# Optimization experiments

Measured on AMD Instinct MI355X. Metric: run time of the kernel, lower is better.

Reference implementation:

```python
import jax, jax.numpy as jnp
import numpy as np

K = 8192          # codebook_size
D = 256           # embedding_dim
BETA = 0.25
DECAY = 0.99
EPS = 1e-5        # EMA eps


def setup_inputs() -> dict:
    key = jax.random.key(0)
    k1, k2 = jax.random.split(key)
    z_e = jax.random.normal(k1, (16, D, 32, 32), dtype=jnp.float32)
    # nn.init.uniform_(weight, -1/K, 1/K)
    weight = jax.random.uniform(k2, (K, D), dtype=jnp.float32, minval=-1.0 / K, maxval=1.0 / K)
    cluster_size = jnp.zeros((K,), dtype=jnp.float32)
    embed_avg = jnp.zeros((K, D), dtype=jnp.float32)
    return {"z_e": z_e, "weight": weight, "cluster_size": cluster_size, "embed_avg": embed_avg}


def reference(z_e, weight, cluster_size, embed_avg):
    B, Dd, H, W = z_e.shape
    flat = z_e.transpose(0, 2, 3, 1).reshape(-1, Dd)          # [N, D]
    codebook = jax.lax.stop_gradient(weight)                    # [K, D]

    # squared L2 distances via expansion (same math as torch source)
    x_sq = jnp.sum(flat * flat, axis=1, keepdims=True)          # [N, 1]
    e_sq = jnp.sum(codebook * codebook, axis=1)[None, :]        # [1, K]
    cross = flat @ codebook.T                                   # [N, K] GEMM
    dist = x_sq + e_sq - 2.0 * cross
    indices = jnp.argmin(dist, axis=1)                          # [N]

    N = flat.shape[0]
    # EMA update (one-hot scatter expressed as segment ops)
    counts = jax.ops.segment_sum(jnp.ones((N,), flat.dtype), indices, num_segments=K)
    embed_sum = jax.ops.segment_sum(flat, indices, num_segments=K)   # [K, D]
    new_cluster = cluster_size * DECAY + counts * (1.0 - DECAY)
    new_embed_avg = embed_avg * DECAY + embed_sum * (1.0 - DECAY)
    n = jnp.sum(new_cluster)
    cs = (new_cluster + EPS) / (n + K * EPS) * n
    new_weight = new_embed_avg / cs[:, None]                    # updated codebook

    # quantize: gather from the UPDATED codebook (as in the torch forward order)
    e = new_weight[indices]                                     # [N, D]
    z_q = e.reshape(B, H, W, Dd).transpose(0, 3, 1, 2)

    commitment_loss = BETA * jnp.mean((z_e - jax.lax.stop_gradient(z_q)) ** 2)
    codebook_loss = jnp.mean((z_q - jax.lax.stop_gradient(z_e)) ** 2)
    usage = counts / N
    return (z_q, commitment_loss, codebook_loss, usage, new_cluster, new_embed_avg)
```

## Files before the change

kernel.cpp:

```cpp
#include <hip/hip_runtime.h>
#include <cstdint>
#include <cstddef>

#define N_TOK   16384
#define K_CODE  8192
#define D_DIM   256
#define HW      1024
#define MARGIN  8e-4f
#define RING    512
#define CAP     990

#define OFF_ZQ   0
#define OFF_CL   4194304
#define OFF_CBL  4194305
#define OFF_USE  4194306
#define OFF_NC   4202498
#define OFF_AVG  4210690

typedef unsigned short ushort_t;
typedef __attribute__((ext_vector_type(8))) short short8;
typedef __attribute__((ext_vector_type(8))) unsigned short ushort8;
typedef __attribute__((ext_vector_type(4))) float f32x4;

__device__ float g_esq[K_CODE];
__device__ float g_xsq[N_TOK];
__device__ __attribute__((aligned(16))) float    g_xf[N_TOK * D_DIM];
__device__ __attribute__((aligned(16))) ushort_t g_xb[N_TOK * D_DIM];
__device__ __attribute__((aligned(16))) ushort_t g_wb[K_CODE * D_DIM];
__device__ int   g_ccnt[N_TOK];
__device__ int   g_cand[N_TOK * RING];
__device__ int   g_idx[N_TOK];
__device__ float g_cnt[K_CODE];
__device__ __attribute__((aligned(16))) float g_esum[K_CODE * D_DIM];
__device__ float g_inv[K_CODE];
__device__ float g_loss[1];

__device__ __forceinline__ ushort_t f2bf(float f) {
  unsigned u = __builtin_bit_cast(unsigned, f);
  return (ushort_t)((u + 0x7FFFu + ((u >> 16) & 1u)) >> 16);
}

__device__ __forceinline__ void gload16(const void* g, void* l) {
  __builtin_amdgcn_global_load_lds(
      (const __attribute__((address_space(1))) unsigned int*)g,
      (__attribute__((address_space(3))) unsigned int*)l, 16, 0, 0);
}

__global__ void k_zero() {
  int i = blockIdx.x * 256 + threadIdx.x;
  if (i < K_CODE) g_cnt[i] = 0.0f;
  if (i < N_TOK) g_ccnt[i] = 0;
  if (i == 0) g_loss[0] = 0.0f;
  for (int j = i; j < K_CODE * D_DIM; j += 524288) g_esum[j] = 0.0f;
}

__global__ void k_esq(const float* __restrict__ wt) {
  int t = threadIdx.x;
  int code = blockIdx.x * 4 + (t >> 6);
  int l = t & 63;
  float4 v = *(const float4*)(wt + (size_t)code * D_DIM + l * 4);
  float s = v.x * v.x + v.y * v.y + v.z * v.z + v.w * v.w;
  #pragma unroll
  for (int m = 1; m < 64; m <<= 1) s += __shfl_xor(s, m, 64);
  if (l == 0) g_esq[code] = s;
}

__global__ void k_split_w(const float* __restrict__ wt) {
  int tg = blockIdx.x * 256 + threadIdx.x;
  int c = tg >> 5, g = tg & 31;
  const float* src = wt + (size_t)c * D_DIM + g * 8;
  float4 v0 = *(const float4*)(src);
  float4 v1 = *(const float4*)(src + 4);
  ushort8 v;
  v[0] = f2bf(v0.x); v[1] = f2bf(v0.y); v[2] = f2bf(v0.z); v[3] = f2bf(v0.w);
  v[4] = f2bf(v1.x); v[5] = f2bf(v1.y); v[6] = f2bf(v1.z); v[7] = f2bf(v1.w);
  *(ushort8*)(g_wb + (size_t)c * D_DIM + ((g ^ (c & 7)) << 3)) = v;
}

__global__ __launch_bounds__(256) void k_prep_x(const float* __restrict__ ze) {
  extern __shared__ char smem[];
  float* T = (float*)smem;
  const int tid = threadIdx.x;
  const int n0 = blockIdx.x * 64;
  const int b = n0 >> 10, hw0 = n0 & 1023;
  const float* zb = ze + (size_t)b * (D_DIM * HW) + hw0;
  #pragma unroll
  for (int p = 0; p < 16; ++p) {
    int idx = p * 256 + tid;
    int d = idx >> 4, f = idx & 15;
    float4 v = *(const float4*)(zb + (size_t)d * HW + f * 4);
    T[(f * 4 + 0) * 260 + d] = v.x;
    T[(f * 4 + 1) * 260 + d] = v.y;
    T[(f * 4 + 2) * 260 + d] = v.z;
    T[(f * 4 + 3) * 260 + d] = v.w;
  }
  __syncthreads();
  if (tid < 64) {
    #pragma clang fp contract(off)
    float s = 0.0f;
    const float* tr = T + tid * 260;
    for (int d = 0; d < D_DIM; ++d) { float v = tr[d]; s = s + v * v; }
    g_xsq[n0 + tid] = s;
  }
  {
    int r = tid >> 2, dc = (tid & 3) * 64;
    const float* tr = T + r * 260 + dc;
    float* dst = g_xf + (size_t)(n0 + r) * D_DIM + dc;
    #pragma unroll
    for (int j = 0; j < 16; ++j) *(float4*)(dst + j * 4) = *(const float4*)(tr + j * 4);
  }
  {
    int r = tid >> 2, gb = (tid & 3) * 8;
    const float* tr = T + r * 260;
    ushort_t* dst = g_xb + (size_t)(n0 + r) * D_DIM;
    int swz = r & 7;
    #pragma unroll
    for (int gg = 0; gg < 8; ++gg) {
      int g = gb + gg;
      ushort8 v;
      #pragma unroll
      for (int j = 0; j < 8; ++j) v[j] = f2bf(tr[g * 8 + j]);
      *(ushort8*)(dst + ((g ^ swz) << 3)) = v;
    }
  }
}

__global__ __launch_bounds__(256, 1) void k_approx1() {
  extern __shared__ char smem[];
  ushort_t* As = (ushort_t*)smem;
  ushort_t* Bs = (ushort_t*)(smem + 32768);
  int* lcnt = (int*)(smem + 65536);

  const int tid = threadIdx.x;
  const int lane = tid & 63, wid = tid >> 6;
  const int col = lane & 15, kg = lane >> 4;
  const int rb = blockIdx.x & 255, sp = blockIdx.x >> 8;
  const int sw = col & 7;
  int* lbuf = (int*)(smem + 65552 + wid * 3960);

  if (tid < 4) lcnt[tid] = 0;

  {
    const char* s = (const char*)g_xb + (size_t)rb * 32768 + wid * 1024 + lane * 16;
    char* d = smem + wid * 1024;
    #pragma unroll
    for (int it = 0; it < 8; ++it) gload16(s + it * 4096, d + it * 4096);
  }
  const char* wsrc = (const char*)g_wb + (size_t)sp * (4096 * 512);
  {
    const char* s = wsrc + wid * 1024 + lane * 16;
    char* d = smem + 32768 + wid * 1024;
    #pragma unroll
    for (int it = 0; it < 4; ++it) gload16(s + it * 4096, d + it * 4096);
  }

  const int rowbase = rb * 64 + wid * 16 + (kg << 2);
  float rm[4], thr[4];
  #pragma unroll
  for (int r = 0; r < 4; ++r) { rm[r] = -1e30f; thr[r] = 1e30f; }

  __syncthreads();

  const int ar0 = (wid * 16 + col) * 256;
  #pragma unroll 1
  for (int ch = 0; ch < 128; ++ch) {
    const int cur = ch & 1;
    const int c0 = sp * 4096 + ch * 32;
    float e0 = g_esq[c0 + col];
    float e1 = g_esq[c0 + 16 + col];
    if (ch < 127) {
      const char* s = wsrc + (size_t)(ch + 1) * 16384 + wid * 1024 + lane * 16;
      char* d = smem + 32768 + ((cur ^ 1) << 14) + wid * 1024;
      #pragma unroll
      for (int it = 0; it < 4; ++it) gload16(s + it * 4096, d + it * 4096);
    }
    const ushort_t* Bb = Bs + (cur << 13);
    f32x4 acc0 = {0.f, 0.f, 0.f, 0.f};
    f32x4 acc1 = {0.f, 0.f, 0.f, 0.f};

    #pragma unroll
    for (int ks = 0; ks < 8; ++ks) {
      const int ko = ((ks * 4 + kg) ^ sw) << 3;
      short8 a  = *(const short8*)(As + ar0 + ko);
      short8 b0 = *(const short8*)(Bb + (col +  0) * 256 + ko);
      short8 b1 = *(const short8*)(Bb + (col + 16) * 256 + ko);
      acc0 = __builtin_amdgcn_mfma_f32_16x16x32_bf16(a, b0, acc0, 0, 0, 0);
      acc1 = __builtin_amdgcn_mfma_f32_16x16x32_bf16(a, b1, acc1, 0, 0, 0);
    }

    float cm[4];
    #pragma unroll
    for (int r = 0; r < 4; ++r) cm[r] = -1e30f;
    #pragma unroll
    for (int n = 0; n < 2; ++n) {
      const int c = c0 + n * 16 + col;
      const float e = n ? e1 : e0;
      const f32x4& a4 = n ? acc1 : acc0;
      #pragma unroll
      for (int r = 0; r < 4; ++r) {
        float sc = fmaf(2.0f, a4[r], -e);
        cm[r] = fmaxf(cm[r], sc);
        if (ch > 0 && sc >= thr[r]) {
          int row = rowbase + r;
          int pos = atomicAdd(&lcnt[wid], 1);
          if (pos < CAP) lbuf[pos] = (row << 13) | c;
          else { int gp = atomicAdd(&g_ccnt[row], 1);
                 if (gp < RING) g_cand[row * RING + gp] = c; }
        }
      }
    }
    #pragma unroll
    for (int mk = 1; mk < 16; mk <<= 1)
      #pragma unroll
      for (int r = 0; r < 4; ++r)
        cm[r] = fmaxf(cm[r], __shfl_xor(cm[r], mk, 64));
    #pragma unroll
    for (int r = 0; r < 4; ++r) {
      rm[r] = fmaxf(rm[r], cm[r]);
      thr[r] = rm[r] - MARGIN;
    }
    if (ch == 0) {
      #pragma unroll
      for (int n = 0; n < 2; ++n) {
        const int c = c0 + n * 16 + col;
        const float e = n ? e1 : e0;
        const f32x4& a4 = n ? acc1 : acc0;
        #pragma unroll
        for (int r = 0; r < 4; ++r) {
          float sc = fmaf(2.0f, a4[r], -e);
          if (sc >= thr[r]) {
            int row = rowbase + r;
            int pos = atomicAdd(&lcnt[wid], 1);
            if (pos < CAP) lbuf[pos] = (row << 13) | c;
            else { int gp = atomicAdd(&g_ccnt[row], 1);
                   if (gp < RING) g_cand[row * RING + gp] = c; }
          }
        }
      }
    }
    __syncthreads();
  }

  __syncthreads();
  int k = lcnt[wid];
  if (k > CAP) k = CAP;
  for (int i = lane; i < k; i += 64) {
    int e = lbuf[i];
    int row = e >> 13, c = e & 8191;
    int pos = atomicAdd(&g_ccnt[row], 1);
    if (pos < RING) g_cand[row * RING + pos] = c;
  }
}

__global__ __launch_bounds__(256) void k_rescore(const float* __restrict__ wt) {
  const int tid = threadIdx.x;
  const int lane = tid & 63, wid = tid >> 6;
  const int n = blockIdx.x * 4 + wid;
  const int grp = lane >> 4;
  const int l15 = lane & 15;
  float4 xf[4];
  const float* xr = g_xf + (size_t)n * D_DIM + l15 * 16;
  #pragma unroll
  for (int j = 0; j < 4; ++j) xf[j] = *(const float4*)(xr + j * 4);
  const float xsq = g_xsq[n];
  const int cnt = g_ccnt[n];
  float bd = INFINITY;
  int bi = 0x7fffffff;

  auto eval4 = [&](int c, bool active) {
    float p = 0.0f;
    if (active) {
      const float* wr = wt + (size_t)c * D_DIM + l15 * 16;
      #pragma unroll
      for (int j = 0; j < 4; ++j) {
        float4 w = *(const float4*)(wr + j * 4);
        p = fmaf(xf[j].x, w.x, p);
        p = fmaf(xf[j].y, w.y, p);
        p = fmaf(xf[j].z, w.z, p);
        p = fmaf(xf[j].w, w.w, p);
      }
    }
    #pragma unroll
    for (int m = 1; m < 16; m <<= 1) p += __shfl_xor(p, m, 64);
    if (active) {
      float d = (xsq + g_esq[c]) - 2.0f * p;
      if (d < bd || (d == bd && c < bi)) { bd = d; bi = c; }
    }
  };

  if (cnt >= 1 && cnt <= RING) {
    for (int i = 0; i < cnt; i += 4) {
      int idx = i + grp;
      bool act = idx < cnt;
      int c = act ? g_cand[n * RING + idx] : 0;
      eval4(c, act);
    }
  } else {
    for (int c0 = 0; c0 < K_CODE; c0 += 4) eval4(c0 + grp, true);
  }
  #pragma unroll
  for (int m = 16; m < 64; m <<= 1) {
    float od = __shfl_xor(bd, m, 64);
    int   oi = __shfl_xor(bi, m, 64);
    if (od < bd || (od == bd && oi < bi)) { bd = od; bi = oi; }
  }
  if (lane == 0) g_idx[n] = bi;
}

__global__ void k_scatter(const float* __restrict__ ze) {
  __shared__ int codes[64];
  int t = threadIdx.x;
  int n0 = blockIdx.x * 64;
  int b = n0 >> 10, hw0 = n0 & 1023;
  if (t < 64) {
    int c = g_idx[n0 + t];
    codes[t] = c;
    atomicAdd(&g_cnt[c], 1.0f);
  }
  __syncthreads();
  int f = t & 15, dd = t >> 4;
  const float* zb = ze + (size_t)b * (D_DIM * HW) + hw0;
  for (int p = 0; p < 16; ++p) {
    int d = p * 16 + dd;
    float4 v = *(const float4*)(zb + (size_t)d * HW + f * 4);
    atomicAdd(&g_esum[codes[4 * f + 0] * D_DIM + d], v.x);
    atomicAdd(&g_esum[codes[4 * f + 1] * D_DIM + d], v.y);
    atomicAdd(&g_esum[codes[4 * f + 2] * D_DIM + d], v.z);
    atomicAdd(&g_esum[codes[4 * f + 3] * D_DIM + d], v.w);
  }
}

__global__ void k_ema(const float* __restrict__ cs_in, float* __restrict__ out) {
  __shared__ float red[4];
  int t = threadIdx.x;
  float local = 0.0f;
  for (int k = t; k < K_CODE; k += 256) local += cs_in[k] * 0.99f + g_cnt[k] * 0.01f;
  #pragma unroll
  for (int m = 1; m < 64; m <<= 1) local += __shfl_xor(local, m, 64);
  if ((t & 63) == 0) red[t >> 6] = local;
  __syncthreads();
  float n = red[0] + red[1] + red[2] + red[3];
  float denom = n + 0.08192f;
  for (int k = t; k < K_CODE; k += 256) {
    float newc = cs_in[k] * 0.99f + g_cnt[k] * 0.01f;
    out[OFF_NC + k]  = newc;
    out[OFF_USE + k] = g_cnt[k] * (1.0f / 16384.0f);
    float cs = ((newc + 1e-5f) / denom) * n;
    g_inv[k] = 1.0f / cs;
  }
}

__global__ void k_avg(const float* __restrict__ ea, float* __restrict__ out) {
  int i = blockIdx.x * 256 + threadIdx.x;
  const float2 a = *(const float2*)(ea + (size_t)i * 2);
  const float2 s = *(const float2*)(g_esum + (size_t)i * 2);
  float2 o;
  o.x = a.x * 0.99f + s.x * 0.01f;
  o.y = a.y * 0.99f + s.y * 0.01f;
  *(float2*)(out + OFF_AVG + (size_t)i * 2) = o;
}

__global__ __launch_bounds__(256) void k_gather(const float* __restrict__ ze,
                                                float* __restrict__ out) {
  __shared__ float W[32 * 260];
  __shared__ int codes[64];
  __shared__ float red[4];
  const float* avg = out + OFF_AVG;
  int t = threadIdx.x;
  int n0 = blockIdx.x * 64;
  int b = n0 >> 10, hw0 = n0 & 1023;
  if (t < 64) codes[t] = g_idx[n0 + t];
  float l = 0.0f;
  const float* zb = ze + (size_t)b * (D_DIM * HW);
  float* qb = out + OFF_ZQ + (size_t)b * (D_DIM * HW);
  for (int pass = 0; pass < 2; ++pass) {
    __syncthreads();
    {
      int rr0 = t >> 6;
      int f = t & 63;
      for (int q = 0; q < 8; ++q) {
        int rr = q * 4 + rr0;
        int c = codes[pass * 32 + rr];
        float iv = g_inv[c];
        float2 w0 = *(const float2*)(avg + (size_t)c * D_DIM + f * 4);
        float2 w1 = *(const float2*)(avg + (size_t)c * D_DIM + f * 4 + 2);
        float* wp = &W[rr * 260 + f * 4];
        wp[0] = w0.x * iv; wp[1] = w0.y * iv; wp[2] = w1.x * iv; wp[3] = w1.y * iv;
      }
    }
    __syncthreads();
    int f = t & 7, dd = t >> 3;
    int hwp = hw0 + pass * 32;
    for (int p = 0; p < 8; ++p) {
      int d = p * 32 + dd;
      float4 zev = *(const float4*)(zb + (size_t)d * HW + hwp + f * 4);
      float4 o;
      o.x = W[(4 * f + 0) * 260 + d];
      o.y = W[(4 * f + 1) * 260 + d];
      o.z = W[(4 * f + 2) * 260 + d];
      o.w = W[(4 * f + 3) * 260 + d];
      *(float4*)(qb + (size_t)d * HW + hwp + f * 4) = o;
      float dx = zev.x - o.x, dy = zev.y - o.y, dz = zev.z - o.z, dw = zev.w - o.w;
      l += dx * dx; l += dy * dy; l += dz * dz; l += dw * dw;
    }
  }
  #pragma unroll
  for (int m = 1; m < 64; m <<= 1) l += __shfl_xor(l, m, 64);
  if ((t & 63) == 0) red[t >> 6] = l;
  __syncthreads();
  if (t == 0) atomicAdd(g_loss, red[0] + red[1] + red[2] + red[3]);
}

__global__ void k_final(float* __restrict__ out) {
  if (threadIdx.x == 0) {
    float mse = g_loss[0] * (1.0f / 4194304.0f);
    out[OFF_CL]  = 0.25f * mse;
    out[OFF_CBL] = mse;
  }
}

extern "C" void kernel_launch(void* const* d_in, const int* in_sizes, int n_in,
                              void* d_out, int out_size, void* d_ws, size_t ws_size,
                              hipStream_t stream) {
  const float* ze    = (const float*)d_in[0];
  const float* wt    = (const float*)d_in[1];
  const float* cs_in = (const float*)d_in[2];
  const float* ea_in = (const float*)d_in[3];
  float* out = (float*)d_out;
  (void)in_sizes; (void)n_in; (void)out_size; (void)d_ws; (void)ws_size;

  (void)hipFuncSetAttribute((const void*)k_prep_x,
                            hipFuncAttributeMaxDynamicSharedMemorySize, 66560);
  (void)hipFuncSetAttribute((const void*)k_approx1,
                            hipFuncAttributeMaxDynamicSharedMemorySize, 81408);

  k_zero<<<2048, 256, 0, stream>>>();
  k_esq<<<K_CODE / 4, 256, 0, stream>>>(wt);
  k_split_w<<<1024, 256, 0, stream>>>(wt);
  k_prep_x<<<N_TOK / 64, 256, 66560, stream>>>(ze);
  k_approx1<<<512, 256, 81408, stream>>>();
  k_rescore<<<N_TOK / 4, 256, 0, stream>>>(wt);
  k_scatter<<<N_TOK / 64, 256, 0, stream>>>(ze);
  k_ema<<<1, 256, 0, stream>>>(cs_in, out);
  k_avg<<<4096, 256, 0, stream>>>(ea_in, out);
  k_gather<<<N_TOK / 64, 256, 0, stream>>>(ze, out);
  k_final<<<1, 64, 0, stream>>>(out);
}
```

Baseline: 463.4 us.

## Hold A fragments in registers and double rows per block in approx GEMM

The approximate distance kernel now keeps each wave's 32 token rows as bf16 MFMA fragments in registers instead of LDS. Each block covers 128 tokens and 2048 codes, so every codebook tile loaded into LDS feeds twice as many MFMAs. The codebook traffic per block halves and LDS use drops. In exchange the kernel needs more VGPRs (16 short8 fragments plus 4 accumulators) and does more per-chunk threshold and shuffle work.

```diff
diff --git a/kernel.cpp b/kernel.cpp
--- a/kernel.cpp
+++ b/kernel.cpp
@@ -127,115 +127,137 @@
 
 __global__ __launch_bounds__(256, 1) void k_approx1() {
   extern __shared__ char smem[];
-  ushort_t* As = (ushort_t*)smem;
-  ushort_t* Bs = (ushort_t*)(smem + 32768);
-  int* lcnt = (int*)(smem + 65536);
-
+  ushort_t* Bs = (ushort_t*)smem;
+  int* lcnt = (int*)(smem + 32768);
   const int tid = threadIdx.x;
   const int lane = tid & 63, wid = tid >> 6;
   const int col = lane & 15, kg = lane >> 4;
-  const int rb = blockIdx.x & 255, sp = blockIdx.x >> 8;
+  const int rb = blockIdx.x & 127, sp = blockIdx.x >> 7;
   const int sw = col & 7;
-  int* lbuf = (int*)(smem + 65552 + wid * 3960);
+  const int rbase = rb * 128 + wid * 32;
+  int* lbuf = (int*)(smem + 32784 + wid * 3960);
 
   if (tid < 4) lcnt[tid] = 0;
 
-  {
-    const char* s = (const char*)g_xb + (size_t)rb * 32768 + wid * 1024 + lane * 16;
-    char* d = smem + wid * 1024;
-    #pragma unroll
-    for (int it = 0; it < 8; ++it) gload16(s + it * 4096, d + it * 4096);
-  }
-  const char* wsrc = (const char*)g_wb + (size_t)sp * (4096 * 512);
+  short8 af[16];
+  #pragma unroll
+  for (int ks = 0; ks < 8; ++ks)
+    #pragma unroll
+    for (int m = 0; m < 2; ++m) {
+      int row = rbase + m * 16 + col;
+      af[ks * 2 + m] = *(const short8*)(g_xb + (size_t)row * 256 + (((ks * 4 + kg) ^ sw) << 3));
+    }
+
+  const char* wsrc = (const char*)g_wb + (size_t)sp * (2048 * 512);
   {
     const char* s = wsrc + wid * 1024 + lane * 16;
-    char* d = smem + 32768 + wid * 1024;
+    char* d = smem + wid * 1024;
     #pragma unroll
     for (int it = 0; it < 4; ++it) gload16(s + it * 4096, d + it * 4096);
   }
 
-  const int rowbase = rb * 64 + wid * 16 + (kg << 2);
-  float rm[4], thr[4];
-  #pragma unroll
-  for (int r = 0; r < 4; ++r) { rm[r] = -1e30f; thr[r] = 1e30f; }
-
-  __syncthreads();
-
-  const int ar0 = (wid * 16 + col) * 256;
+  float rm[2][4], thr[2][4];
+  #pragma unroll
+  for (int m = 0; m < 2; ++m)
+    #pragma unroll
+    for (int r = 0; r < 4; ++r) { rm[m][r] = -1e30f; thr[m][r] = 1e30f; }
+
+  __syncthreads();
+
   #pragma unroll 1
-  for (int ch = 0; ch < 128; ++ch) {
+  for (int ch = 0; ch < 64; ++ch) {
     const int cur = ch & 1;
-    const int c0 = sp * 4096 + ch * 32;
+    const int c0 = sp * 2048 + ch * 32;
     float e0 = g_esq[c0 + col];
     float e1 = g_esq[c0 + 16 + col];
-    if (ch < 127) {
+    if (ch < 63) {
       const char* s = wsrc + (size_t)(ch + 1) * 16384 + wid * 1024 + lane * 16;
-      char* d = smem + 32768 + ((cur ^ 1) << 14) + wid * 1024;
+      char* d = smem + ((cur ^ 1) << 14) + wid * 1024;
       #pragma unroll
       for (int it = 0; it < 4; ++it) gload16(s + it * 4096, d + it * 4096);
     }
     const ushort_t* Bb = Bs + (cur << 13);
-    f32x4 acc0 = {0.f, 0.f, 0.f, 0.f};
-    f32x4 acc1 = {0.f, 0.f, 0.f, 0.f};
+    f32x4 acc[2][2];
+    const f32x4 zero4 = {0.f, 0.f, 0.f, 0.f};
+    #pragma unroll
+    for (int m = 0; m < 2; ++m)
+      #pragma unroll
+      for (int n = 0; n < 2; ++n) acc[m][n] = zero4;
 
     #pragma unroll
     for (int ks = 0; ks < 8; ++ks) {
       const int ko = ((ks * 4 + kg) ^ sw) << 3;
-      short8 a  = *(const short8*)(As + ar0 + ko);
       short8 b0 = *(const short8*)(Bb + (col +  0) * 256 + ko);
       short8 b1 = *(const short8*)(Bb + (col + 16) * 256 + ko);
-      acc0 = __builtin_amdgcn_mfma_f32_16x16x32_bf16(a, b0, acc0, 0, 0, 0);
-      acc1 = __builtin_amdgcn_mfma_f32_16x16x32_bf16(a, b1, acc1, 0, 0, 0);
-    }
-
-    float cm[4];
-    #pragma unroll
-    for (int r = 0; r < 4; ++r) cm[r] = -1e30f;
+      acc[0][0] = __builtin_amdgcn_mfma_f32_16x16x32_bf16(af[ks*2+0], b0, acc[0][0], 0, 0, 0);
+      acc[1][0] = __builtin_amdgcn_mfma_f32_16x16x32_bf16(af[ks*2+1], b0, acc[1][0], 0, 0, 0);
+      acc[0][1] = __builtin_amdgcn_mfma_f32_16x16x32_bf16(af[ks*2+0], b1, acc[0][1], 0, 0, 0);
+      acc[1][1] = __builtin_amdgcn_mfma_f32_16x16x32_bf16(af[ks*2+1], b1, acc[1][1], 0, 0, 0);
+    }
+
+    float cm[2][4], sv[2][2][4];
+    #pragma unroll
+    for (int m = 0; m < 2; ++m)
+      #pragma unroll
+      for (int r = 0; r < 4; ++r) cm[m][r] = -1e30f;
     #pragma unroll
     for (int n = 0; n < 2; ++n) {
-      const int c = c0 + n * 16 + col;
       const float e = n ? e1 : e0;
-      const f32x4& a4 = n ? acc1 : acc0;
-      #pragma unroll
-      for (int r = 0; r < 4; ++r) {
-        float sc = fmaf(2.0f, a4[r], -e);
-        cm[r] = fmaxf(cm[r], sc);
-        if (ch > 0 && sc >= thr[r]) {
-          int row = rowbase + r;
-          int pos = atomicAdd(&lcnt[wid], 1);
-          if (pos < CAP) lbuf[pos] = (row << 13) | c;
-          else { int gp = atomicAdd(&g_ccnt[row], 1);
-                 if (gp < RING) g_cand[row * RING + gp] = c; }
+      #pragma unroll
+      for (int m = 0; m < 2; ++m)
+        #pragma unroll
+        for (int r = 0; r < 4; ++r) {
+          float sc = fmaf(2.0f, acc[m][n][r], -e);
+          sv[m][n][r] = sc;
+          cm[m][r] = fmaxf(cm[m][r], sc);
         }
-      }
-    }
-    #pragma unroll
-    for (int mk = 1; mk < 16; mk <<= 1)
-      #pragma unroll
-      for (int r = 0; r < 4; ++r)
-        cm[r] = fmaxf(cm[r], __shfl_xor(cm[r], mk, 64));
-    #pragma unroll
-    for (int r = 0; r < 4; ++r) {
-      rm[r] = fmaxf(rm[r], cm[r]);
-      thr[r] = rm[r] - MARGIN;
-    }
-    if (ch == 0) {
+    }
+    if (ch > 0) {
       #pragma unroll
       for (int n = 0; n < 2; ++n) {
         const int c = c0 + n * 16 + col;
-        const float e = n ? e1 : e0;
-        const f32x4& a4 = n ? acc1 : acc0;
         #pragma unroll
-        for (int r = 0; r < 4; ++r) {
-          float sc = fmaf(2.0f, a4[r], -e);
-          if (sc >= thr[r]) {
-            int row = rowbase + r;
-            int pos = atomicAdd(&lcnt[wid], 1);
-            if (pos < CAP) lbuf[pos] = (row << 13) | c;
-            else { int gp = atomicAdd(&g_ccnt[row], 1);
-                   if (gp < RING) g_cand[row * RING + gp] = c; }
-          }
-        }
+        for (int m = 0; m < 2; ++m)
+          #pragma unroll
+          for (int r = 0; r < 4; ++r)
+            if (sv[m][n][r] >= thr[m][r]) {
+              int row = rbase + m * 16 + (kg << 2) + r;
+              int pos = atomicAdd(&lcnt[wid], 1);
+              if (pos < CAP) lbuf[pos] = (row << 13) | c;
+              else { int gp = atomicAdd(&g_ccnt[row], 1);
+                     if (gp < RING) g_cand[row * RING + gp] = c; }
+            }
+      }
+    }
+    #pragma unroll
+    for (int mk = 1; mk < 16; mk <<= 1)
+      #pragma unroll
+      for (int m = 0; m < 2; ++m)
+        #pragma unroll
+        for (int r = 0; r < 4; ++r)
+          cm[m][r] = fmaxf(cm[m][r], __shfl_xor(cm[m][r], mk, 64));
+    #pragma unroll
+    for (int m = 0; m < 2; ++m)
+      #pragma unroll
+      for (int r = 0; r < 4; ++r) {
+        rm[m][r] = fmaxf(rm[m][r], cm[m][r]);
+        thr[m][r] = rm[m][r] - MARGIN;
+      }
+    if (ch == 0) {
+      #pragma unroll
+      for (int n = 0; n < 2; ++n) {
+        const int c = c0 + n * 16 + col;
+        #pragma unroll
+        for (int m = 0; m < 2; ++m)
+          #pragma unroll
+          for (int r = 0; r < 4; ++r)
+            if (sv[m][n][r] >= thr[m][r]) {
+              int row = rbase + m * 16 + (kg << 2) + r;
+              int pos = atomicAdd(&lcnt[wid], 1);
+              if (pos < CAP) lbuf[pos] = (row << 13) | c;
+              else { int gp = atomicAdd(&g_ccnt[row], 1);
+                     if (gp < RING) g_cand[row * RING + gp] = c; }
+            }
       }
     }
     __syncthreads();
@@ -432,13 +454,13 @@
   (void)hipFuncSetAttribute((const void*)k_prep_x,
                             hipFuncAttributeMaxDynamicSharedMemorySize, 66560);
   (void)hipFuncSetAttribute((const void*)k_approx1,
-                            hipFuncAttributeMaxDynamicSharedMemorySize, 81408);
+                            hipFuncAttributeMaxDynamicSharedMemorySize, 48640);
 
   k_zero<<<2048, 256, 0, stream>>>();
   k_esq<<<K_CODE / 4, 256, 0, stream>>>(wt);
   k_split_w<<<1024, 256, 0, stream>>>(wt);
   k_prep_x<<<N_TOK / 64, 256, 66560, stream>>>(ze);
-  k_approx1<<<512, 256, 81408, stream>>>();
+  k_approx1<<<512, 256, 48640, stream>>>();
   k_rescore<<<N_TOK / 4, 256, 0, stream>>>(wt);
   k_scatter<<<N_TOK / 64, 256, 0, stream>>>(ze);
   k_ema<<<1, 256, 0, stream>>>(cs_in, out);
```

Measured after the change: 455.8 us. No clear change (-1.6%).
